# Optimization experiments

Hardware: AMD Instinct MI355X
Metric: run time of the kernel (lower is better)

Reference implementation:

```python
import jax, jax.numpy as jnp
import numpy as np

N_GAUSS = 512
PLANE = 512


def setup_inputs() -> dict:
    key = jax.random.key(0)
    k1, k2, k3, k4, k5 = jax.random.split(key, 5)
    mean = jax.random.uniform(k1, (N_GAUSS, 2, 1), dtype=jnp.float32)
    alpha = jax.random.uniform(k2, (N_GAUSS, 1), dtype=jnp.float32)
    scale = jax.random.uniform(k3, (N_GAUSS, 2), dtype=jnp.float32)
    theta = jax.random.uniform(k4, (N_GAUSS, 1), dtype=jnp.float32)
    rgb = jax.random.uniform(k5, (N_GAUSS, 3), dtype=jnp.float32)
    # render plane: torch.meshgrid(x, y, indexing='xy'), stack([x, y], -1)
    lin = jnp.linspace(0.0, 1.0, PLANE, dtype=jnp.float32)
    xx, yy = jnp.meshgrid(lin, lin, indexing='xy')
    pixels = jnp.stack([xx, yy], axis=-1)  # (H, W, 2)
    return {"mean": mean, "alpha": alpha, "scale": scale, "theta": theta,
            "rgb": rgb, "pixels": pixels}


def _forward(mean, alpha, scale, theta, rgb, pixels):
    two_pi = 2.0 * jnp.pi
    # covariance = R S S^T R^T with R from circular_activation(theta)
    ta = two_pi * theta                      # (N,1)
    c = jnp.cos(ta)
    s = jnp.sin(ta)
    rot = jnp.stack([jnp.concatenate([c, -s], axis=-1),
                     jnp.concatenate([s, c], axis=-1)], axis=-2)   # (N,2,2)
    smat = jnp.eye(2, dtype=scale.dtype)[None] * scale[..., None]  # (N,2,2)
    cov = rot @ smat @ jnp.swapaxes(smat, -1, -2) @ jnp.swapaxes(rot, -1, -2)
    a = cov[:, 0, 0]
    b01 = cov[:, 0, 1]
    b10 = cov[:, 1, 0]
    d = cov[:, 1, 1]
    det = a * d - b01 * b10                  # (N,)
    inv00 = d / det
    inv01 = -b01 / det
    inv10 = -b10 / det
    inv11 = a / det
    # quadratic form per pixel (analytic 2x2, same math as diff^T inv diff)
    mu = mean[:, :, 0]                       # (N,2)
    dx = pixels[None, :, :, 0] - mu[:, 0][:, None, None]  # (N,H,W)
    dy = pixels[None, :, :, 1] - mu[:, 1][:, None, None]  # (N,H,W)
    q = (inv00[:, None, None] * dx * dx
         + (inv01 + inv10)[:, None, None] * dx * dy
         + inv11[:, None, None] * dy * dy)
    prob = jnp.exp(-0.5 * q) / (two_pi * jnp.sqrt(det))[:, None, None]  # (N,H,W)
    splat = prob / jnp.max(prob)             # global max-normalize
    weighted = rgb * alpha                   # (N,3) rgb * alpha mask
    img = jnp.einsum('nhw,nc->hwc', splat, weighted)  # sum over gaussians
    return jax.nn.sigmoid(img)               # (H,W,3)


def reference(mean, alpha, scale, theta, rgb, pixels):
    return _forward(mean, alpha, scale, theta, rgb, pixels)
```

## Files before the change

### kernel.cpp

```cpp
#include <hip/hip_runtime.h>

#define NG 512
#define PLANE 512

typedef float v2f __attribute__((ext_vector_type(2)));

#define PRM_OFF  16
#define SLOT_OFF 4352

__global__ __launch_bounds__(256) void prep_kernel(
    const float* __restrict__ mean, const float* __restrict__ alpha,
    const float* __restrict__ scale, const float* __restrict__ theta,
    const float* __restrict__ rgb, float* __restrict__ ws) {
    const int n   = blockIdx.x;
    const int tid = threadIdx.x;

    const float TWO_PI = 6.283185307179586f;
    float th = theta[n];
    float c = __builtin_amdgcn_cosf(th);
    float s = __builtin_amdgcn_sinf(th);
    float sx = scale[2 * n], sy = scale[2 * n + 1];

    float m200 = (c * sx) * sx;
    float m201 = (-(s * sy)) * sy;
    float m210 = (s * sx) * sx;
    float m211 = (c * sy) * sy;
    float a   = m200 * c + m201 * (-s);
    float b01 = m200 * s + m201 * c;
    float b10 = m210 * c + m211 * (-s);
    float d   = m210 * s + m211 * c;

    float det = a * d - b01 * b10;
    float rdet = __builtin_amdgcn_rcpf(det);
    float inv00 = d * rdet;
    float inv01 = -b01 * rdet;
    float inv10 = -b10 * rdet;
    float inv11 = a * rdet;

    float norm = __builtin_amdgcn_rcpf(TWO_PI * __builtin_amdgcn_sqrtf(det));
    const float K = -0.5f * 1.4426950408889634f;

    float A_ = K * inv00;
    float B_ = K * (inv01 + inv10);
    float C_ = K * inv11;
    float mx = mean[2 * n], my = mean[2 * n + 1];
    float Lg = fmaf(-0.5f, __builtin_amdgcn_logf(det), -2.651496129472319f);

    if (tid == 0) {
        float w = alpha[n] * norm;
        float4* p = (float4*)(ws + PRM_OFF + 8 * n);
        p[0] = make_float4(A_, B_, C_, mx);
        p[1] = make_float4(my, w * rgb[3 * n], w * rgb[3 * n + 1], w * rgb[3 * n + 2]);
    }

    const float STEP = 1.0f / 511.0f;
    float inv2A = __builtin_amdgcn_rcpf(2.0f * A_);
    float t = -1e30f;
#pragma unroll
    for (int k = 0; k < 2; ++k) {
        int r = tid + (k << 8);
        float y  = (float)r * STEP;
        float dy = y - my;
        float bdy  = B_ * dy;
        float cdy2 = C_ * (dy * dy);
        float xstar = mx - bdy * inv2A;
        float xs = fminf(fmaxf(xstar, 0.0f), 1.0f);
        int i1 = min((int)(xs * 511.0f), 510);
#pragma unroll
        for (int kk = -1; kk <= 2; ++kk) {
            int i = max(0, min(i1 + kk, 511));
            float x = (float)i * STEP;
            float dx = x - mx;
            float q = fmaf(fmaf(A_, dx, bdy), dx, cdy2);
            t = fmaxf(t, q);
        }
    }
    t += Lg;

#pragma unroll
    for (int off = 32; off > 0; off >>= 1)
        t = fmaxf(t, __shfl_xor(t, off));
    __shared__ float sm[4];
    if ((tid & 63) == 0) sm[tid >> 6] = t;
    __syncthreads();
    if (tid == 0) {
        float mm = fmaxf(fmaxf(sm[0], sm[1]), fmaxf(sm[2], sm[3]));
        ws[SLOT_OFF + n] = mm;
    }
}

__global__ __launch_bounds__(512, 2) void splat_kernel(
    const float* __restrict__ pixels, const float* __restrict__ ws,
    float* __restrict__ out) {
    const int tid  = threadIdx.x;
    const int wv   = __builtin_amdgcn_readfirstlane(tid >> 6);
    const int lane = tid & 63;
    const int row  = blockIdx.x;
    const int px0  = (row << 9) + (lane << 3);

    const float4* pp = reinterpret_cast<const float4*>(pixels + 2 * px0);
    float4 pA = pp[0], pB = pp[1], pC = pp[2], pD = pp[3];
    const float y = pA.y;
    const v2f x01 = {pA.x, pA.z};
    const v2f x23 = {pB.x, pB.z};
    const v2f x45 = {pC.x, pC.z};
    const v2f x67 = {pD.x, pD.z};

    const float4* prm4 = reinterpret_cast<const float4*>(ws + PRM_OFF) + (wv << 7);

    v2f ar01 = {0.f, 0.f}, ag01 = {0.f, 0.f}, ab01 = {0.f, 0.f};
    v2f ar23 = {0.f, 0.f}, ag23 = {0.f, 0.f}, ab23 = {0.f, 0.f};
    v2f ar45 = {0.f, 0.f}, ag45 = {0.f, 0.f}, ab45 = {0.f, 0.f};
    v2f ar67 = {0.f, 0.f}, ag67 = {0.f, 0.f}, ab67 = {0.f, 0.f};

#pragma unroll 4
    for (int n = 0; n < 64; ++n) {
        float4 pa = prm4[2 * n];
        float4 pb = prm4[2 * n + 1];

        float a = pa.x, b = pa.y, cc = pa.z, mx = pa.w;
        float my = pb.x, wr = pb.y, wg = pb.z, wb = pb.w;

        float dy   = y - my;
        float bdy  = b * dy;
        float cdy2 = cc * (dy * dy);
        v2f av    = {a, a};
        v2f mxv   = {mx, mx};
        v2f bdyv  = {bdy, bdy};
        v2f cdy2v = {cdy2, cdy2};

        v2f dx01 = x01 - mxv, dx23 = x23 - mxv, dx45 = x45 - mxv, dx67 = x67 - mxv;
        v2f t01 = __builtin_elementwise_fma(dx01, av, bdyv);
        v2f t23 = __builtin_elementwise_fma(dx23, av, bdyv);
        v2f t45 = __builtin_elementwise_fma(dx45, av, bdyv);
        v2f t67 = __builtin_elementwise_fma(dx67, av, bdyv);
        v2f q01 = __builtin_elementwise_fma(t01, dx01, cdy2v);
        v2f q23 = __builtin_elementwise_fma(t23, dx23, cdy2v);
        v2f q45 = __builtin_elementwise_fma(t45, dx45, cdy2v);
        v2f q67 = __builtin_elementwise_fma(t67, dx67, cdy2v);

        v2f e01 = {__builtin_amdgcn_exp2f(q01.x), __builtin_amdgcn_exp2f(q01.y)};
        v2f e23 = {__builtin_amdgcn_exp2f(q23.x), __builtin_amdgcn_exp2f(q23.y)};
        v2f e45 = {__builtin_amdgcn_exp2f(q45.x), __builtin_amdgcn_exp2f(q45.y)};
        v2f e67 = {__builtin_amdgcn_exp2f(q67.x), __builtin_amdgcn_exp2f(q67.y)};

        v2f wrv = {wr, wr}, wgv = {wg, wg}, wbv = {wb, wb};
        ar01 = __builtin_elementwise_fma(e01, wrv, ar01);
        ag01 = __builtin_elementwise_fma(e01, wgv, ag01);
        ab01 = __builtin_elementwise_fma(e01, wbv, ab01);
        ar23 = __builtin_elementwise_fma(e23, wrv, ar23);
        ag23 = __builtin_elementwise_fma(e23, wgv, ag23);
        ab23 = __builtin_elementwise_fma(e23, wbv, ab23);
        ar45 = __builtin_elementwise_fma(e45, wrv, ar45);
        ag45 = __builtin_elementwise_fma(e45, wgv, ag45);
        ab45 = __builtin_elementwise_fma(e45, wbv, ab45);
        ar67 = __builtin_elementwise_fma(e67, wrv, ar67);
        ag67 = __builtin_elementwise_fma(e67, wgv, ag67);
        ab67 = __builtin_elementwise_fma(e67, wbv, ab67);
    }

    float invmax;
    {
        const float4* sl = reinterpret_cast<const float4*>(ws + SLOT_OFF) + 2 * lane;
        float4 s0 = sl[0], s1 = sl[1];
        float m = fmaxf(fmaxf(fmaxf(s0.x, s0.y), fmaxf(s0.z, s0.w)),
                        fmaxf(fmaxf(s1.x, s1.y), fmaxf(s1.z, s1.w)));
#pragma unroll
        for (int off = 32; off > 0; off >>= 1)
            m = fmaxf(m, __shfl_xor(m, off));
        invmax = __builtin_amdgcn_exp2f(-m);
    }

    __shared__ float4 red[8][64][6];
    red[wv][lane][0] = make_float4(ar01.x, ag01.x, ab01.x, ar01.y);
    red[wv][lane][1] = make_float4(ag01.y, ab01.y, ar23.x, ag23.x);
    red[wv][lane][2] = make_float4(ab23.x, ar23.y, ag23.y, ab23.y);
    red[wv][lane][3] = make_float4(ar45.x, ag45.x, ab45.x, ar45.y);
    red[wv][lane][4] = make_float4(ag45.y, ab45.y, ar67.x, ag67.x);
    red[wv][lane][5] = make_float4(ab67.x, ar67.y, ag67.y, ab67.y);
    __syncthreads();

    if (tid < 384) {
        const int l    = tid / 6;
        const int slot = tid - 6 * l;
        float4 v = red[0][l][slot];
#pragma unroll
        for (int cch = 1; cch < 8; ++cch) {
            float4 u = red[cch][l][slot];
            v.x += u.x; v.y += u.y; v.z += u.z; v.w += u.w;
        }
        const float KE = 1.4426950408889634f;
#define SIG(x) __builtin_amdgcn_rcpf(1.0f + __builtin_amdgcn_exp2f(-KE * ((x) * invmax)))
        v.x = SIG(v.x); v.y = SIG(v.y); v.z = SIG(v.z); v.w = SIG(v.w);
#undef SIG
        reinterpret_cast<float4*>(out)[row * 384 + tid] = v;
    }
}

extern "C" void kernel_launch(void* const* d_in, const int* in_sizes, int n_in,
                              void* d_out, int out_size, void* d_ws, size_t ws_size,
                              hipStream_t stream) {
    const float* mean   = (const float*)d_in[0];
    const float* alpha  = (const float*)d_in[1];
    const float* scale  = (const float*)d_in[2];
    const float* theta  = (const float*)d_in[3];
    const float* rgb    = (const float*)d_in[4];
    const float* pixels = (const float*)d_in[5];
    float* out = (float*)d_out;
    float* ws  = (float*)d_ws;

    prep_kernel<<<512, 256, 0, stream>>>(mean, alpha, scale, theta, rgb, ws);

    splat_kernel<<<512, 512, 0, stream>>>(pixels, ws, out);
}
```

Baseline: 91.97 us.

## Precompute per-row per-gaussian quadratic coefficients in prep kernel table

The prep kernel now runs one block per image row with one thread per gaussian. Each thread writes a per-(row, gaussian) table entry holding A, beta, gamma and the weighted rgb, recentred at x=0.5. The splat kernel then evaluates the quadratic with two FMAs per pixel and drops the per-gaussian dy/bdy/cdy2 work. It also software-prefetches the next table entry. In exchange this adds an 8 MB workspace table that must be written and read back, raising memory traffic, and the per-gaussian max is now computed per row instead.

```diff
diff --git a/kernel.cpp b/kernel.cpp
--- a/kernel.cpp
+++ b/kernel.cpp
@@ -5,15 +5,15 @@
 
 typedef float v2f __attribute__((ext_vector_type(2)));
 
-#define PRM_OFF  16
 #define SLOT_OFF 4352
-
-__global__ __launch_bounds__(256) void prep_kernel(
+#define TBL_OFF  8192
+
+__global__ __launch_bounds__(512) void prep_kernel(
     const float* __restrict__ mean, const float* __restrict__ alpha,
     const float* __restrict__ scale, const float* __restrict__ theta,
     const float* __restrict__ rgb, float* __restrict__ ws) {
-    const int n   = blockIdx.x;
-    const int tid = threadIdx.x;
+    const int row = blockIdx.x;
+    const int n   = threadIdx.x;
 
     const float TWO_PI = 6.283185307179586f;
     float th = theta[n];
@@ -45,47 +45,48 @@
     float C_ = K * inv11;
     float mx = mean[2 * n], my = mean[2 * n + 1];
     float Lg = fmaf(-0.5f, __builtin_amdgcn_logf(det), -2.651496129472319f);
-
-    if (tid == 0) {
-        float w = alpha[n] * norm;
-        float4* p = (float4*)(ws + PRM_OFF + 8 * n);
-        p[0] = make_float4(A_, B_, C_, mx);
-        p[1] = make_float4(my, w * rgb[3 * n], w * rgb[3 * n + 1], w * rgb[3 * n + 2]);
-    }
+    float w  = alpha[n] * norm;
 
     const float STEP = 1.0f / 511.0f;
+    float y  = (float)row * STEP;
+    float dy = y - my;
+    float bdy  = B_ * dy;
+    float cdy2 = C_ * (dy * dy);
+
+    float mxp   = mx - 0.5f;
+    float beta  = fmaf(-2.0f * A_, mxp, bdy);
+    float gamma = fmaf(fmaf(A_, mxp, -bdy), mxp, cdy2);
+
+    float4* te = (float4*)(ws + TBL_OFF + ((size_t)(row << 9) + n) * 8);
+    te[0] = make_float4(A_, beta, gamma, w * rgb[3 * n]);
+    te[1] = make_float4(w * rgb[3 * n + 1], w * rgb[3 * n + 2], 0.f, 0.f);
+
     float inv2A = __builtin_amdgcn_rcpf(2.0f * A_);
+    float xstar = mx - bdy * inv2A;
+    float xs = fminf(fmaxf(xstar, 0.0f), 1.0f);
+    int i1 = min((int)(xs * 511.0f), 510);
     float t = -1e30f;
 #pragma unroll
-    for (int k = 0; k < 2; ++k) {
-        int r = tid + (k << 8);
-        float y  = (float)r * STEP;
-        float dy = y - my;
-        float bdy  = B_ * dy;
-        float cdy2 = C_ * (dy * dy);
-        float xstar = mx - bdy * inv2A;
-        float xs = fminf(fmaxf(xstar, 0.0f), 1.0f);
-        int i1 = min((int)(xs * 511.0f), 510);
-#pragma unroll
-        for (int kk = -1; kk <= 2; ++kk) {
-            int i = max(0, min(i1 + kk, 511));
-            float x = (float)i * STEP;
-            float dx = x - mx;
-            float q = fmaf(fmaf(A_, dx, bdy), dx, cdy2);
-            t = fmaxf(t, q);
-        }
+    for (int kk = -1; kk <= 2; ++kk) {
+        int i = max(0, min(i1 + kk, 511));
+        float x = (float)i * STEP;
+        float dx = x - mx;
+        float q = fmaf(fmaf(A_, dx, bdy), dx, cdy2);
+        t = fmaxf(t, q);
     }
     t += Lg;
 
 #pragma unroll
     for (int off = 32; off > 0; off >>= 1)
         t = fmaxf(t, __shfl_xor(t, off));
-    __shared__ float sm[4];
-    if ((tid & 63) == 0) sm[tid >> 6] = t;
+    __shared__ float sm[8];
+    if ((n & 63) == 0) sm[n >> 6] = t;
     __syncthreads();
-    if (tid == 0) {
-        float mm = fmaxf(fmaxf(sm[0], sm[1]), fmaxf(sm[2], sm[3]));
-        ws[SLOT_OFF + n] = mm;
+    if (n == 0) {
+        float mm = sm[0];
+#pragma unroll
+        for (int wv2 = 1; wv2 < 8; ++wv2) mm = fmaxf(mm, sm[wv2]);
+        ws[SLOT_OFF + row] = mm;
     }
 }
 
@@ -100,44 +101,39 @@
 
     const float4* pp = reinterpret_cast<const float4*>(pixels + 2 * px0);
     float4 pA = pp[0], pB = pp[1], pC = pp[2], pD = pp[3];
-    const float y = pA.y;
-    const v2f x01 = {pA.x, pA.z};
-    const v2f x23 = {pB.x, pB.z};
-    const v2f x45 = {pC.x, pC.z};
-    const v2f x67 = {pD.x, pD.z};
-
-    const float4* prm4 = reinterpret_cast<const float4*>(ws + PRM_OFF) + (wv << 7);
+    const v2f half2 = {0.5f, 0.5f};
+    const v2f u01 = (v2f){pA.x, pA.z} - half2;
+    const v2f u23 = (v2f){pB.x, pB.z} - half2;
+    const v2f u45 = (v2f){pC.x, pC.z} - half2;
+    const v2f u67 = (v2f){pD.x, pD.z} - half2;
+
+    const float4* tbl = reinterpret_cast<const float4*>(ws + TBL_OFF)
+                        + ((size_t)row << 10) + (wv << 7);
 
     v2f ar01 = {0.f, 0.f}, ag01 = {0.f, 0.f}, ab01 = {0.f, 0.f};
     v2f ar23 = {0.f, 0.f}, ag23 = {0.f, 0.f}, ab23 = {0.f, 0.f};
     v2f ar45 = {0.f, 0.f}, ag45 = {0.f, 0.f}, ab45 = {0.f, 0.f};
     v2f ar67 = {0.f, 0.f}, ag67 = {0.f, 0.f}, ab67 = {0.f, 0.f};
 
+    float4 ta = tbl[0];
+    float4 tb = tbl[1];
 #pragma unroll 4
     for (int n = 0; n < 64; ++n) {
-        float4 pa = prm4[2 * n];
-        float4 pb = prm4[2 * n + 1];
-
-        float a = pa.x, b = pa.y, cc = pa.z, mx = pa.w;
-        float my = pb.x, wr = pb.y, wg = pb.z, wb = pb.w;
-
-        float dy   = y - my;
-        float bdy  = b * dy;
-        float cdy2 = cc * (dy * dy);
-        v2f av    = {a, a};
-        v2f mxv   = {mx, mx};
-        v2f bdyv  = {bdy, bdy};
-        v2f cdy2v = {cdy2, cdy2};
-
-        v2f dx01 = x01 - mxv, dx23 = x23 - mxv, dx45 = x45 - mxv, dx67 = x67 - mxv;
-        v2f t01 = __builtin_elementwise_fma(dx01, av, bdyv);
-        v2f t23 = __builtin_elementwise_fma(dx23, av, bdyv);
-        v2f t45 = __builtin_elementwise_fma(dx45, av, bdyv);
-        v2f t67 = __builtin_elementwise_fma(dx67, av, bdyv);
-        v2f q01 = __builtin_elementwise_fma(t01, dx01, cdy2v);
-        v2f q23 = __builtin_elementwise_fma(t23, dx23, cdy2v);
-        v2f q45 = __builtin_elementwise_fma(t45, dx45, cdy2v);
-        v2f q67 = __builtin_elementwise_fma(t67, dx67, cdy2v);
+        float4 na = tbl[2 * n + 2];
+        float4 nb = tbl[2 * n + 3];
+
+        float A_ = ta.x, beta = ta.y, gamma = ta.z, wr = ta.w;
+        float wg = tb.x, wb = tb.y;
+        v2f Av = {A_, A_}, bev = {beta, beta}, gav = {gamma, gamma};
+
+        v2f t01 = __builtin_elementwise_fma(u01, Av, bev);
+        v2f t23 = __builtin_elementwise_fma(u23, Av, bev);
+        v2f t45 = __builtin_elementwise_fma(u45, Av, bev);
+        v2f t67 = __builtin_elementwise_fma(u67, Av, bev);
+        v2f q01 = __builtin_elementwise_fma(t01, u01, gav);
+        v2f q23 = __builtin_elementwise_fma(t23, u23, gav);
+        v2f q45 = __builtin_elementwise_fma(t45, u45, gav);
+        v2f q67 = __builtin_elementwise_fma(t67, u67, gav);
 
         v2f e01 = {__builtin_amdgcn_exp2f(q01.x), __builtin_amdgcn_exp2f(q01.y)};
         v2f e23 = {__builtin_amdgcn_exp2f(q23.x), __builtin_amdgcn_exp2f(q23.y)};
@@ -157,6 +153,8 @@
         ar67 = __builtin_elementwise_fma(e67, wrv, ar67);
         ag67 = __builtin_elementwise_fma(e67, wgv, ag67);
         ab67 = __builtin_elementwise_fma(e67, wbv, ab67);
+
+        ta = na; tb = nb;
     }
 
     float invmax;
@@ -209,7 +207,7 @@
     float* out = (float*)d_out;
     float* ws  = (float*)d_ws;
 
-    prep_kernel<<<512, 256, 0, stream>>>(mean, alpha, scale, theta, rgb, ws);
+    prep_kernel<<<512, 512, 0, stream>>>(mean, alpha, scale, theta, rgb, ws);
 
     splat_kernel<<<512, 512, 0, stream>>>(pixels, ws, out);
 }
```

Result: slower. 94.04 us (+2.2%).
